# Performance work log

Measured on AMD Instinct MI355X. Metric: run time of the kernel, lower is better.

## Reference

```python
import jax, jax.numpy as jnp
import numpy as np

N, M, H, K, CIN, COUT, P = 50000, 50000, 32, 15, 64, 128, 3
KP_EXTENT = 0.072
RADIUS = 0.06


def setup_inputs() -> dict:
    key = jax.random.key(0)
    ks = jax.random.split(key, 7)
    q_pts = jax.random.uniform(ks[0], (N, P), dtype=jnp.float32) * 0.05
    s_pts = jax.random.uniform(ks[1], (M, P), dtype=jnp.float32) * 0.05
    neighb_inds = jax.random.randint(ks[2], (N, H), 0, M, dtype=jnp.int64)
    x = jax.random.normal(ks[3], (M, CIN), dtype=jnp.float32)
    # kernel points inside sphere of radius RADIUS (stand-in for load_kernels)
    kernel_points = jax.random.normal(ks[4], (K, P), dtype=jnp.float32) * (0.5 * RADIUS)
    stddev = np.sqrt(1.0 / (K * COUT)).astype(np.float32)
    weights = jax.random.normal(ks[5], (K, CIN, COUT), dtype=jnp.float32) * stddev
    bias = jnp.zeros((COUT,), dtype=jnp.float32)
    return {"q_pts": q_pts, "s_pts": s_pts, "neighb_inds": neighb_inds,
            "x": x, "kernel_points": kernel_points, "weights": weights, "bias": bias}


def reference(q_pts, s_pts, neighb_inds, x, kernel_points, weights, bias):
    # pad support points with a far-away point and features with a zero row
    s_pad = jnp.concatenate([s_pts, jnp.full((1, s_pts.shape[1]), 1e6, s_pts.dtype)], axis=0)
    x_pad = jnp.concatenate([x, jnp.zeros((1, x.shape[1]), x.dtype)], axis=0)
    # gather neighbor coords/features: [N, H, P], [N, H, CIN]
    neighbors = s_pad[neighb_inds] - q_pts[:, None, :]
    neighb_x = x_pad[neighb_inds]
    # distances to kernel points: [N, H, K]
    diff = neighbors[:, :, None, :] - kernel_points  # [N, H, K, P]
    sq_d = jnp.sum(diff * diff, axis=-1)
    all_weights = jax.nn.relu(1.0 - jnp.sqrt(sq_d) / KP_EXTENT)  # linear influence
    # aggregate: [N, K, CIN] then apply per-kernel-point weights and sum over K
    weighted_features = jnp.einsum('nhk,nhc->nkc', all_weights, neighb_x)
    out = jnp.einsum('nkc,kco->no', weighted_features, weights) + bias  # [N, COUT]
    return out
```

## Files before the change

### kernel.cpp

```cpp
#include <hip/hip_runtime.h>
#include <hip/hip_bf16.h>


#define NPTS   50000
#define NPAD   50048
#define HNB    32
#define KPTS   15
#define CING   64
#define COUTG  128
#define KDIM   960
#define MSUP   50000
#define INV_EXT 13.888889f

typedef __attribute__((ext_vector_type(8))) short bf16x8;
typedef __attribute__((ext_vector_type(8))) unsigned short u16x8;
typedef __attribute__((ext_vector_type(4))) float f32x4;

static __device__ __forceinline__ unsigned short f2bf(float f) {
    unsigned int u = __float_as_uint(f);
    u += 0x7FFFu + ((u >> 16) & 1u);
    return (unsigned short)(u >> 16);
}

__global__ __launch_bounds__(256) void kpconv_x2bf(const float* __restrict__ x,
                                                   unsigned short* __restrict__ xb) {
    int i = (blockIdx.x * 256 + threadIdx.x) * 8;
    if (i >= MSUP * CING) return;
    float4 a = *(const float4*)(x + i);
    float4 b = *(const float4*)(x + i + 4);
    u16x8 o;
    o[0] = f2bf(a.x); o[1] = f2bf(a.y); o[2] = f2bf(a.z); o[3] = f2bf(a.w);
    o[4] = f2bf(b.x); o[5] = f2bf(b.y); o[6] = f2bf(b.z); o[7] = f2bf(b.w);
    *(u16x8*)(xb + i) = o;
}

__global__ void kpconv_wt(const float* __restrict__ wgt, unsigned short* __restrict__ Wt) {
    int kc = blockIdx.x;
    int o  = threadIdx.x;
    Wt[(size_t)o * KDIM + kc] = f2bf(wgt[(size_t)kc * COUTG + o]);
}

__global__ __launch_bounds__(256) void kpconv_agg2(
    const float* __restrict__ q_pts, const float* __restrict__ s_pts,
    const int* __restrict__ inds, const unsigned short* __restrict__ xb,
    const float* __restrict__ kpts, unsigned short* __restrict__ wf)
{
    __shared__ float4 nb4[4][HNB];

    const int tid  = threadIdx.x;
    const int g    = tid >> 6;
    const int lane = tid & 63;
    const int l15  = lane & 15;
    const int quad = lane >> 4;
    const int n    = blockIdx.x * 4 + g;

    if (lane < HNB) {
        int m = inds[n * HNB + lane];
        float qx = q_pts[n * 3 + 0];
        float qy = q_pts[n * 3 + 1];
        float qz = q_pts[n * 3 + 2];
        nb4[g][lane] = make_float4(s_pts[m * 3 + 0] - qx,
                                   s_pts[m * 3 + 1] - qy,
                                   s_pts[m * 3 + 2] - qz,
                                   __int_as_float(m));
    }
    __syncthreads();

    const bool kvalid = (l15 < KPTS);
    const int  kidx   = kvalid ? l15 : 0;
    const float kx = kpts[kidx * 3 + 0];
    const float ky = kpts[kidx * 3 + 1];
    const float kz = kpts[kidx * 3 + 2];

    bf16x8 af;
    int mrow[8];
#pragma unroll
    for (int j = 0; j < 8; ++j) {
        float4 v = nb4[g][quad * 8 + j];
        mrow[j] = __float_as_int(v.w);
        float dx = v.x - kx, dy = v.y - ky, dz = v.z - kz;
        float d  = sqrtf(dx * dx + dy * dy + dz * dz);
        float w  = kvalid ? fmaxf(0.f, 1.f - d * INV_EXT) : 0.f;
        af[j] = (short)f2bf(w);
    }

    f32x4 acc[4];
#pragma unroll
    for (int nt = 0; nt < 4; ++nt) acc[nt] = (f32x4){0.f, 0.f, 0.f, 0.f};

#pragma unroll
    for (int nt = 0; nt < 4; ++nt) {
        const int c = nt * 16 + l15;
        bf16x8 bfr;
#pragma unroll
        for (int j = 0; j < 8; ++j)
            bfr[j] = (short)xb[((size_t)mrow[j] << 6) + c];
        acc[nt] = __builtin_amdgcn_mfma_f32_16x16x32_bf16(af, bfr, acc[nt], 0, 0, 0);
    }

    const size_t base = (size_t)n * KDIM;
#pragma unroll
    for (int nt = 0; nt < 4; ++nt) {
        const int c = nt * 16 + l15;
#pragma unroll
        for (int r = 0; r < 4; ++r) {
            int k = quad * 4 + r;
            if (k < KPTS) wf[base + k * CING + c] = f2bf(acc[nt][r]);
        }
    }
}

#define GBM 64
#define GBK 64
#define GLP 72

__global__ __launch_bounds__(256) void kpconv_gemm2(
    const unsigned short* __restrict__ A,
    const unsigned short* __restrict__ Bt,
    const float* __restrict__ bias,
    float* __restrict__ out)
{
    __shared__ unsigned short As[GBM * GLP];
    __shared__ unsigned short Bs[COUTG * GLP];

    const int tid  = threadIdx.x;
    const int wave = tid >> 6;
    const int lane = tid & 63;
    const int l15  = lane & 15;
    const int quad = lane >> 4;
    const long blockM = (long)blockIdx.x * GBM;

    f32x4 acc[8];
#pragma unroll
    for (int i = 0; i < 8; ++i) acc[i] = (f32x4){0.f, 0.f, 0.f, 0.f};

    const int arow = tid >> 2, acol = (tid & 3) * 16;
    const int brow = tid >> 1, bcol = (tid & 1) * 32;
    const unsigned short* aptr = A + (size_t)(blockM + arow) * KDIM + acol;
    const unsigned short* bptr = Bt + (size_t)brow * KDIM + bcol;

    uint4 ra0 = *(const uint4*)(aptr);
    uint4 ra1 = *(const uint4*)(aptr + 8);
    uint4 rb0 = *(const uint4*)(bptr);
    uint4 rb1 = *(const uint4*)(bptr + 8);
    uint4 rb2 = *(const uint4*)(bptr + 16);
    uint4 rb3 = *(const uint4*)(bptr + 24);

    for (int kk = 0; kk < KDIM; kk += GBK) {
        __syncthreads();
        *(uint4*)&As[arow * GLP + acol]      = ra0;
        *(uint4*)&As[arow * GLP + acol + 8]  = ra1;
        *(uint4*)&Bs[brow * GLP + bcol]      = rb0;
        *(uint4*)&Bs[brow * GLP + bcol + 8]  = rb1;
        *(uint4*)&Bs[brow * GLP + bcol + 16] = rb2;
        *(uint4*)&Bs[brow * GLP + bcol + 24] = rb3;
        __syncthreads();

        if (kk + GBK < KDIM) {
            ra0 = *(const uint4*)(aptr + kk + GBK);
            ra1 = *(const uint4*)(aptr + kk + GBK + 8);
            rb0 = *(const uint4*)(bptr + kk + GBK);
            rb1 = *(const uint4*)(bptr + kk + GBK + 8);
            rb2 = *(const uint4*)(bptr + kk + GBK + 16);
            rb3 = *(const uint4*)(bptr + kk + GBK + 24);
        }

#pragma unroll
        for (int ch = 0; ch < 2; ++ch) {
            bf16x8 afr = *(bf16x8*)&As[(wave * 16 + l15) * GLP + ch * 32 + quad * 8];
#pragma unroll
            for (int nf = 0; nf < 8; ++nf) {
                bf16x8 bfr = *(bf16x8*)&Bs[(nf * 16 + l15) * GLP + ch * 32 + quad * 8];
                acc[nf] = __builtin_amdgcn_mfma_f32_16x16x32_bf16(afr, bfr, acc[nf], 0, 0, 0);
            }
        }
    }

    const long r0 = blockM + wave * 16 + quad * 4;
#pragma unroll
    for (int nf = 0; nf < 8; ++nf) {
        const int col = nf * 16 + l15;
        const float bv = bias[col];
#pragma unroll
        for (int r = 0; r < 4; ++r) {
            long row = r0 + r;
            if (row < NPTS) out[row * COUTG + col] = acc[nf][r] + bv;
        }
    }
}

extern "C" void kernel_launch(void* const* d_in, const int* in_sizes, int n_in,
                              void* d_out, int out_size, void* d_ws, size_t ws_size,
                              hipStream_t stream) {
    const float* q_pts = (const float*)d_in[0];
    const float* s_pts = (const float*)d_in[1];
    const int*   inds  = (const int*)d_in[2];
    const float* x     = (const float*)d_in[3];
    const float* kpts  = (const float*)d_in[4];
    const float* wgt   = (const float*)d_in[5];
    const float* bias  = (const float*)d_in[6];
    float* out = (float*)d_out;

    unsigned short* wf = (unsigned short*)d_ws;
    unsigned short* xb = wf + (size_t)NPAD * KDIM;
    unsigned short* Wt = xb + (size_t)MSUP * CING;

    kpconv_x2bf<<<(MSUP * CING / 8 + 255) / 256, 256, 0, stream>>>(x, xb);
    kpconv_wt<<<KDIM, COUTG, 0, stream>>>(wgt, Wt);
    kpconv_agg2<<<NPTS / 4, 256, 0, stream>>>(q_pts, s_pts, inds, xb, kpts, wf);
    kpconv_gemm2<<<NPAD / GBM, 256, 0, stream>>>(wf, Wt, bias, out);
}
```

Before: 161.0 us.

## Fuse neighbor aggregation and output GEMM into one kernel via LDS tile

Merges the aggregation kernel and the weight GEMM into a single kernel. Each block handles 16 points: it builds the weighted-feature tile (16x960 bf16) in swizzled shared memory, then multiplies it by the transposed weights, which are read directly from global/L2. This drops the ~96MB bf16 intermediate written and re-read through HBM. In exchange, weights are re-streamed per block from cache, and the MFMA operand order is swapped so the tile is transposed.

```diff
diff --git a/kernel.cpp b/kernel.cpp
--- a/kernel.cpp
+++ b/kernel.cpp
@@ -1,9 +1,7 @@
 #include <hip/hip_runtime.h>
-#include <hip/hip_bf16.h>
 
 
 #define NPTS   50000
-#define NPAD   50048
 #define HNB    32
 #define KPTS   15
 #define CING   64
@@ -11,6 +9,9 @@
 #define KDIM   960
 #define MSUP   50000
 #define INV_EXT 13.888889f
+
+#define PPB      16
+#define WF_PITCH 968
 
 typedef __attribute__((ext_vector_type(8))) short bf16x8;
 typedef __attribute__((ext_vector_type(8))) unsigned short u16x8;
@@ -40,29 +41,35 @@
     Wt[(size_t)o * KDIM + kc] = f2bf(wgt[(size_t)kc * COUTG + o]);
 }
 
-__global__ __launch_bounds__(256) void kpconv_agg2(
+__global__ __launch_bounds__(256, 4) void kpconv_fused(
     const float* __restrict__ q_pts, const float* __restrict__ s_pts,
     const int* __restrict__ inds, const unsigned short* __restrict__ xb,
-    const float* __restrict__ kpts, unsigned short* __restrict__ wf)
+    const float* __restrict__ kpts, const unsigned short* __restrict__ Wt,
+    const float* __restrict__ bias, float* __restrict__ out)
 {
-    __shared__ float4 nb4[4][HNB];
+    __shared__ float4 nb[PPB * HNB];
+    __shared__ unsigned short wfs[PPB * WF_PITCH];
 
     const int tid  = threadIdx.x;
-    const int g    = tid >> 6;
+    const int wav  = tid >> 6;
     const int lane = tid & 63;
     const int l15  = lane & 15;
     const int quad = lane >> 4;
-    const int n    = blockIdx.x * 4 + g;
+    const int p0   = blockIdx.x * PPB;
 
-    if (lane < HNB) {
-        int m = inds[n * HNB + lane];
+#pragma unroll
+    for (int t = 0; t < 2; ++t) {
+        int pid = t * 256 + tid;
+        int p = pid >> 5, h = pid & 31;
+        int n = p0 + p;
+        int m = inds[n * HNB + h];
         float qx = q_pts[n * 3 + 0];
         float qy = q_pts[n * 3 + 1];
         float qz = q_pts[n * 3 + 2];
-        nb4[g][lane] = make_float4(s_pts[m * 3 + 0] - qx,
-                                   s_pts[m * 3 + 1] - qy,
-                                   s_pts[m * 3 + 2] - qz,
-                                   __int_as_float(m));
+        nb[pid] = make_float4(s_pts[m * 3 + 0] - qx,
+                              s_pts[m * 3 + 1] - qy,
+                              s_pts[m * 3 + 2] - qz,
+                              __int_as_float(m));
     }
     __syncthreads();
 
@@ -72,119 +79,70 @@
     const float ky = kpts[kidx * 3 + 1];
     const float kz = kpts[kidx * 3 + 2];
 
-    bf16x8 af;
-    int mrow[8];
+#pragma unroll 1
+    for (int pp = 0; pp < 4; ++pp) {
+        const int p = wav * 4 + pp;
+        bf16x8 af;
+        const unsigned short* xr[8];
 #pragma unroll
-    for (int j = 0; j < 8; ++j) {
-        float4 v = nb4[g][quad * 8 + j];
-        mrow[j] = __float_as_int(v.w);
-        float dx = v.x - kx, dy = v.y - ky, dz = v.z - kz;
-        float d  = sqrtf(dx * dx + dy * dy + dz * dz);
-        float w  = kvalid ? fmaxf(0.f, 1.f - d * INV_EXT) : 0.f;
-        af[j] = (short)f2bf(w);
-    }
+        for (int j = 0; j < 8; ++j) {
+            float4 v = nb[p * HNB + quad * 8 + j];
+            int m = __float_as_int(v.w);
+            xr[j] = xb + (((size_t)m) << 6) + l15;
+            float dx = v.x - kx, dy = v.y - ky, dz = v.z - kz;
+            float d  = sqrtf(dx * dx + dy * dy + dz * dz);
+            float w  = kvalid ? fmaxf(0.f, 1.f - d * INV_EXT) : 0.f;
+            af[j] = (short)f2bf(w);
+        }
 
-    f32x4 acc[4];
+        f32x4 acc[4];
 #pragma unroll
-    for (int nt = 0; nt < 4; ++nt) acc[nt] = (f32x4){0.f, 0.f, 0.f, 0.f};
+        for (int nt = 0; nt < 4; ++nt) acc[nt] = (f32x4){0.f, 0.f, 0.f, 0.f};
 
 #pragma unroll
-    for (int nt = 0; nt < 4; ++nt) {
-        const int c = nt * 16 + l15;
-        bf16x8 bfr;
+        for (int nt = 0; nt < 4; ++nt) {
+            bf16x8 bfr;
 #pragma unroll
-        for (int j = 0; j < 8; ++j)
-            bfr[j] = (short)xb[((size_t)mrow[j] << 6) + c];
-        acc[nt] = __builtin_amdgcn_mfma_f32_16x16x32_bf16(af, bfr, acc[nt], 0, 0, 0);
-    }
-
-    const size_t base = (size_t)n * KDIM;
-#pragma unroll
-    for (int nt = 0; nt < 4; ++nt) {
-        const int c = nt * 16 + l15;
-#pragma unroll
-        for (int r = 0; r < 4; ++r) {
-            int k = quad * 4 + r;
-            if (k < KPTS) wf[base + k * CING + c] = f2bf(acc[nt][r]);
-        }
-    }
-}
-
-#define GBM 64
-#define GBK 64
-#define GLP 72
-
-__global__ __launch_bounds__(256) void kpconv_gemm2(
-    const unsigned short* __restrict__ A,
-    const unsigned short* __restrict__ Bt,
-    const float* __restrict__ bias,
-    float* __restrict__ out)
-{
-    __shared__ unsigned short As[GBM * GLP];
-    __shared__ unsigned short Bs[COUTG * GLP];
-
-    const int tid  = threadIdx.x;
-    const int wave = tid >> 6;
-    const int lane = tid & 63;
-    const int l15  = lane & 15;
-    const int quad = lane >> 4;
-    const long blockM = (long)blockIdx.x * GBM;
-
-    f32x4 acc[8];
-#pragma unroll
-    for (int i = 0; i < 8; ++i) acc[i] = (f32x4){0.f, 0.f, 0.f, 0.f};
-
-    const int arow = tid >> 2, acol = (tid & 3) * 16;
-    const int brow = tid >> 1, bcol = (tid & 1) * 32;
-    const unsigned short* aptr = A + (size_t)(blockM + arow) * KDIM + acol;
-    const unsigned short* bptr = Bt + (size_t)brow * KDIM + bcol;
-
-    uint4 ra0 = *(const uint4*)(aptr);
-    uint4 ra1 = *(const uint4*)(aptr + 8);
-    uint4 rb0 = *(const uint4*)(bptr);
-    uint4 rb1 = *(const uint4*)(bptr + 8);
-    uint4 rb2 = *(const uint4*)(bptr + 16);
-    uint4 rb3 = *(const uint4*)(bptr + 24);
-
-    for (int kk = 0; kk < KDIM; kk += GBK) {
-        __syncthreads();
-        *(uint4*)&As[arow * GLP + acol]      = ra0;
-        *(uint4*)&As[arow * GLP + acol + 8]  = ra1;
-        *(uint4*)&Bs[brow * GLP + bcol]      = rb0;
-        *(uint4*)&Bs[brow * GLP + bcol + 8]  = rb1;
-        *(uint4*)&Bs[brow * GLP + bcol + 16] = rb2;
-        *(uint4*)&Bs[brow * GLP + bcol + 24] = rb3;
-        __syncthreads();
-
-        if (kk + GBK < KDIM) {
-            ra0 = *(const uint4*)(aptr + kk + GBK);
-            ra1 = *(const uint4*)(aptr + kk + GBK + 8);
-            rb0 = *(const uint4*)(bptr + kk + GBK);
-            rb1 = *(const uint4*)(bptr + kk + GBK + 8);
-            rb2 = *(const uint4*)(bptr + kk + GBK + 16);
-            rb3 = *(const uint4*)(bptr + kk + GBK + 24);
+            for (int j = 0; j < 8; ++j) bfr[j] = (short)xr[j][nt * 16];
+            acc[nt] = __builtin_amdgcn_mfma_f32_16x16x32_bf16(bfr, af, acc[nt], 0, 0, 0);
         }
 
+        if (kvalid) {
+            char* rowp = (char*)wfs + p * (WF_PITCH * 2);
 #pragma unroll
-        for (int ch = 0; ch < 2; ++ch) {
-            bf16x8 afr = *(bf16x8*)&As[(wave * 16 + l15) * GLP + ch * 32 + quad * 8];
-#pragma unroll
-            for (int nf = 0; nf < 8; ++nf) {
-                bf16x8 bfr = *(bf16x8*)&Bs[(nf * 16 + l15) * GLP + ch * 32 + quad * 8];
-                acc[nf] = __builtin_amdgcn_mfma_f32_16x16x32_bf16(afr, bfr, acc[nf], 0, 0, 0);
+            for (int nt = 0; nt < 4; ++nt) {
+                unsigned int lo = (unsigned)f2bf(acc[nt][0]) | ((unsigned)f2bf(acc[nt][1]) << 16);
+                unsigned int hi = (unsigned)f2bf(acc[nt][2]) | ((unsigned)f2bf(acc[nt][3]) << 16);
+                const int off = (l15 * 128 + nt * 32 + quad * 8) ^ ((l15 & 7) << 4);
+                *(uint2*)(rowp + off) = make_uint2(lo, hi);
             }
         }
     }
+    __syncthreads();
 
-    const long r0 = blockM + wave * 16 + quad * 4;
+    f32x4 oacc[2];
+    oacc[0] = (f32x4){0.f, 0.f, 0.f, 0.f};
+    oacc[1] = (f32x4){0.f, 0.f, 0.f, 0.f};
+    const unsigned short* b0 = Wt + (size_t)(wav * 32 + l15) * KDIM + quad * 8;
+
 #pragma unroll
-    for (int nf = 0; nf < 8; ++nf) {
-        const int col = nf * 16 + l15;
+    for (int s = 0; s < 30; ++s) {
+        const int aoff = (s * 64 + quad * 16) ^ (((s >> 1) & 7) << 4);
+        bf16x8 afr = *(const bf16x8*)((const char*)wfs + l15 * (WF_PITCH * 2) + aoff);
+        bf16x8 w0 = *(const bf16x8*)(b0 + s * 32);
+        bf16x8 w1 = *(const bf16x8*)(b0 + 16 * KDIM + s * 32);
+        oacc[0] = __builtin_amdgcn_mfma_f32_16x16x32_bf16(afr, w0, oacc[0], 0, 0, 0);
+        oacc[1] = __builtin_amdgcn_mfma_f32_16x16x32_bf16(afr, w1, oacc[1], 0, 0, 0);
+    }
+
+#pragma unroll
+    for (int nf = 0; nf < 2; ++nf) {
+        const int col = wav * 32 + nf * 16 + l15;
         const float bv = bias[col];
 #pragma unroll
         for (int r = 0; r < 4; ++r) {
-            long row = r0 + r;
-            if (row < NPTS) out[row * COUTG + col] = acc[nf][r] + bv;
+            const long row = (long)p0 + quad * 4 + r;
+            out[row * COUTG + col] = oacc[nf][r] + bv;
         }
     }
 }
@@ -201,12 +159,10 @@
     const float* bias  = (const float*)d_in[6];
     float* out = (float*)d_out;
 
-    unsigned short* wf = (unsigned short*)d_ws;
-    unsigned short* xb = wf + (size_t)NPAD * KDIM;
+    unsigned short* xb = (unsigned short*)d_ws;
     unsigned short* Wt = xb + (size_t)MSUP * CING;
 
     kpconv_x2bf<<<(MSUP * CING / 8 + 255) / 256, 256, 0, stream>>>(x, xb);
     kpconv_wt<<<KDIM, COUTG, 0, stream>>>(wgt, Wt);
-    kpconv_agg2<<<NPTS / 4, 256, 0, stream>>>(q_pts, s_pts, inds, xb, kpts, wf);
-    kpconv_gemm2<<<NPAD / GBM, 256, 0, stream>>>(wf, Wt, bias, out);
+    kpconv_fused<<<NPTS / PPB, 256, 0, stream>>>(q_pts, s_pts, inds, xb, kpts, Wt, bias, out);
 }
```

New measurement: 206.3 us. 1.28x slower.
